# Optimization experiments

Measured on AMD Instinct MI355X. Metric: run time of the kernel, lower is better.

## Reference

```python
import jax, jax.numpy as jnp
import numpy as np

D_LATENT = 8
N_CENTERS = 48
CHANNELS = 64
PM_STEPS = 4
DT, BETA, CLAMP = 0.12, 1.0, 3.0
SIGMA_E, SIGMA_I, K_E, K_I, GAIN = 0.6, 1.2, 0.8, 1.0, 0.06


def setup_inputs() -> dict:
    key = jax.random.key(0)
    ks = jax.random.split(key, 12)
    B = 8192
    x = jax.random.normal(ks[0], (B, 784), dtype=jnp.float32)
    # encoder params (torch Linear default-ish init scale)
    W1 = jax.random.normal(ks[1], (784, 256), dtype=jnp.float32) * (1.0 / np.sqrt(784))
    b1 = jnp.zeros((256,), jnp.float32)
    W2 = jax.random.normal(ks[2], (256, D_LATENT), dtype=jnp.float32) * (1.0 / np.sqrt(256))
    b2 = jnp.zeros((D_LATENT,), jnp.float32)
    centers = jax.random.normal(ks[3], (N_CENTERS, D_LATENT), dtype=jnp.float32) * 0.7
    mus = jnp.ones((N_CENTERS,), jnp.float32) * 0.4
    projW = jax.random.normal(ks[4], (D_LATENT, CHANNELS), dtype=jnp.float32) * (1.0 / np.sqrt(D_LATENT))
    projb = jnp.zeros((CHANNELS,), jnp.float32)
    roW = jax.random.normal(ks[5], (CHANNELS, 10), dtype=jnp.float32) * (1.0 / np.sqrt(CHANNELS))
    rob = jnp.zeros((10,), jnp.float32)
    return {"x": x, "W1": W1, "b1": b1, "W2": W2, "b2": b2,
            "centers": centers, "mus": mus, "projW": projW, "projb": projb,
            "roW": roW, "rob": rob, "T": 5}


def _pm_field(z, centers, mus):
    # one PMField forward: `PM_STEPS` gradient-flow steps on z [B, d]
    for _ in range(PM_STEPS):
        diff = z[:, None, :] - centers[None, :, :]            # [B, C, d]
        r2 = jnp.sum(diff * diff, axis=-1) + 1e-4              # [B, C]
        r = jnp.sqrt(r2)
        n = 1.0 + jnp.sum(mus[None, :] / r, axis=1)            # [B]
        g = -jnp.sum(mus[None, :, None] * diff / (r * r2)[:, :, None], axis=1)  # [B, d]
        z = z + DT * BETA * (g / n[:, None])
        z = jnp.clip(z, -CLAMP, CLAMP)
    return z


def _lateral_ei(z, h):
    # kernel computed with no_grad in torch -> stop_gradient here
    sq = jnp.sum(z * z, axis=1)                                # [B]
    dist2 = jnp.maximum(sq[:, None] + sq[None, :] - 2.0 * (z @ z.T), 0.0)
    Ke = K_E * jnp.exp(-dist2 / (2.0 * SIGMA_E ** 2))
    Ki = K_I * jnp.exp(-dist2 / (2.0 * SIGMA_I ** 2))
    K = Ke - Ki
    K = K / (jnp.sum(K, axis=1, keepdims=True) + 1e-6)
    K = jax.lax.stop_gradient(K)
    return GAIN * (K @ h)


def reference(x, W1, b1, W2, b2, centers, mus, projW, projb, roW, rob, T):
    z = jnp.tanh(x @ W1 + b1) @ W2 + b2                        # encoder -> [B, d]
    h = jnp.zeros((x.shape[0], CHANNELS), x.dtype)
    logits = None
    for _ in range(T):
        z = _pm_field(z, centers, mus)
        h = 0.9 * h + 0.1 * jnp.tanh(z @ projW + projb)
        h = h + _lateral_ei(z, h)
        logits = h @ roW + rob
    return logits, z, h
```

## Files before the change

kernel.cpp:

```cpp
#include <hip/hip_runtime.h>
#include <hip/hip_bf16.h>
#include <math.h>

#define B_N      8192
#define IN_DIM   784
#define HID      256
#define DL       8
#define NC       48
#define CH       64
#define NCLS     10
#define T_ITERS  5
#define TILES    128

#define DT_      0.12f
#define CLAMP_   3.0f
#define GAIN_    0.06f
#define SQIL2    0.70776814f
#define ONE_BF16 0x3F80u

#if defined(__has_builtin)
#if __has_builtin(__builtin_amdgcn_exp2f)
#define EXP2(x) __builtin_amdgcn_exp2f(x)
#endif
#endif
#ifndef EXP2
#define EXP2(x) exp2f(x)
#endif

typedef __attribute__((ext_vector_type(8))) short short8v;
typedef __attribute__((ext_vector_type(4))) float f32x4;

__device__ __forceinline__ unsigned int pack_bf16_rhu(float lo, float hi) {
    unsigned int b0 = __builtin_bit_cast(unsigned int, lo);
    unsigned int b1 = __builtin_bit_cast(unsigned int, hi);
    return ((b0 + 0x8000u) >> 16) | ((b1 + 0x8000u) & 0xFFFF0000u);
}
__device__ __forceinline__ unsigned short bf16_1(float x) {
    return (unsigned short)((__builtin_bit_cast(unsigned int, x) + 0x8000u) >> 16);
}
__device__ __forceinline__ float bf16_to_f(unsigned short h) {
    return __builtin_bit_cast(float, ((unsigned int)h) << 16);
}

__device__ __forceinline__ void z_split(const float4 a, const float4 b,
                                        uint4& Whi, uint4& Wlo, unsigned int& Wc)
{
    float u[8] = {SQIL2*a.x, SQIL2*a.y, SQIL2*a.z, SQIL2*a.w,
                  SQIL2*b.x, SQIL2*b.y, SQIL2*b.z, SQIL2*b.w};
    float sq = 0.f;
    #pragma unroll
    for (int d = 0; d < 8; ++d) sq = fmaf(u[d], u[d], sq);
    float cn = -0.5f * sq;
    unsigned short hi[8]; float lo[8];
    #pragma unroll
    for (int d = 0; d < 8; ++d) {
        hi[d] = bf16_1(u[d]);
        lo[d] = u[d] - bf16_to_f(hi[d]);
    }
    unsigned short ch_ = bf16_1(cn);
    unsigned short cl_ = bf16_1(cn - bf16_to_f(ch_));
    Whi.x = (unsigned int)hi[0] | ((unsigned int)hi[1] << 16);
    Whi.y = (unsigned int)hi[2] | ((unsigned int)hi[3] << 16);
    Whi.z = (unsigned int)hi[4] | ((unsigned int)hi[5] << 16);
    Whi.w = (unsigned int)hi[6] | ((unsigned int)hi[7] << 16);
    Wlo.x = pack_bf16_rhu(lo[0], lo[1]); Wlo.y = pack_bf16_rhu(lo[2], lo[3]);
    Wlo.z = pack_bf16_rhu(lo[4], lo[5]); Wlo.w = pack_bf16_rhu(lo[6], lo[7]);
    Wc = (unsigned int)ch_ | ((unsigned int)cl_ << 16);
}

__global__ __launch_bounds__(256) void k_gemm1_tanh(
    const float* __restrict__ x, const float* __restrict__ W1,
    const float* __restrict__ b1, float* __restrict__ H1)
{
    __shared__ float As[2][16][68];
    __shared__ float Bs[2][16][64];
    const int tid = threadIdx.x;
    const int row0 = blockIdx.x * 64;
    const int col0 = blockIdx.y * 64;
    const int tr = tid >> 4, tc = tid & 15;
    const int am = tid >> 2, akq = tid & 3;
    const int bkk = tid >> 4, bn4 = tid & 15;
    float acc[4][4] = {};

    {
        float4 va = *(const float4*)(x + (size_t)(row0 + am) * IN_DIM + akq * 4);
        float4 vb = *(const float4*)(W1 + (size_t)bkk * HID + col0 + bn4 * 4);
        As[0][akq*4+0][am] = va.x; As[0][akq*4+1][am] = va.y;
        As[0][akq*4+2][am] = va.z; As[0][akq*4+3][am] = va.w;
        *(float4*)(&Bs[0][bkk][bn4*4]) = vb;
    }

    const int NK = IN_DIM / 16;
    #pragma unroll 1
    for (int ks = 0; ks < NK; ++ks) {
        const int cur = ks & 1;
        const bool more = (ks + 1 < NK);
        float4 va, vb;
        if (more) {
            const int k0 = (ks + 1) * 16;
            va = *(const float4*)(x + (size_t)(row0 + am) * IN_DIM + k0 + akq * 4);
            vb = *(const float4*)(W1 + (size_t)(k0 + bkk) * HID + col0 + bn4 * 4);
        }
        __syncthreads();
        #pragma unroll
        for (int kk = 0; kk < 16; ++kk) {
            float4 a = *(const float4*)(&As[cur][kk][tr*4]);
            float4 b = *(const float4*)(&Bs[cur][kk][tc*4]);
            float av[4] = {a.x, a.y, a.z, a.w};
            float bv[4] = {b.x, b.y, b.z, b.w};
            #pragma unroll
            for (int i = 0; i < 4; ++i)
                #pragma unroll
                for (int j = 0; j < 4; ++j)
                    acc[i][j] += av[i] * bv[j];
        }
        if (more) {
            const int nb = cur ^ 1;
            As[nb][akq*4+0][am] = va.x; As[nb][akq*4+1][am] = va.y;
            As[nb][akq*4+2][am] = va.z; As[nb][akq*4+3][am] = va.w;
            *(float4*)(&Bs[nb][bkk][bn4*4]) = vb;
        }
    }

    const float4 b1c = *(const float4*)(b1 + col0 + tc * 4);
    const float bb[4] = {b1c.x, b1c.y, b1c.z, b1c.w};
    #pragma unroll
    for (int i = 0; i < 4; ++i) {
        int r = row0 + tr*4 + i;
        float4 hv;
        hv.x = tanhf(acc[i][0] + bb[0]);
        hv.y = tanhf(acc[i][1] + bb[1]);
        hv.z = tanhf(acc[i][2] + bb[2]);
        hv.w = tanhf(acc[i][3] + bb[3]);
        *(float4*)(H1 + (size_t)r * HID + col0 + tc * 4) = hv;
    }
}

__global__ __launch_bounds__(256) void k_gemm2(
    const float* __restrict__ H1, const float* __restrict__ W2,
    const float* __restrict__ b2, float* __restrict__ zbuf)
{
    __shared__ float W2s[HID][DL];
    const int tid = threadIdx.x;
    for (int l = tid; l < HID * DL; l += 256) W2s[l >> 3][l & 7] = W2[l];
    __syncthreads();
    const int row = blockIdx.x * 32 + (tid >> 3);
    const int d = tid & 7;
    float acc = b2[d];
    const float* hr = H1 + (size_t)row * HID;
    for (int k = 0; k < HID; k += 4) {
        float4 hv = *(const float4*)(hr + k);
        acc += hv.x * W2s[k][d] + hv.y * W2s[k+1][d]
             + hv.z * W2s[k+2][d] + hv.w * W2s[k+3][d];
    }
    zbuf[(size_t)row * DL + d] = acc;
}

template<int S, bool HP>
__global__ __launch_bounds__(256) void k_pm_proj(
    const float* __restrict__ centers, const float* __restrict__ mus,
    const float* __restrict__ projW, const float* __restrict__ projb,
    float* __restrict__ zbuf, float* __restrict__ hB,
    unsigned short* __restrict__ hTb,
    const float* __restrict__ pAcc, const float* __restrict__ pDen)
{
    __shared__ float4 cs4[NC][2];
    __shared__ float mu_s[NC];
    __shared__ float pW[DL][CH];
    __shared__ float pb[CH];
    const int tid = threadIdx.x;
    for (int l = tid; l < NC * 2; l += 256) cs4[l >> 1][l & 1] = ((const float4*)centers)[l];
    if (tid < NC) mu_s[tid] = mus[tid];
    for (int l = tid; l < DL * CH; l += 256) pW[l >> 6][l & 63] = projW[l];
    if (tid < CH) pb[tid] = projb[tid];
    __syncthreads();

    const int rloc = tid >> 4;
    const int ln   = tid & 15;
    const int row  = blockIdx.x * 16 + rloc;

    float4 cza[3], czb[3];
    float mur[3];
    #pragma unroll
    for (int k = 0; k < 3; ++k) {
        cza[k] = cs4[ln + 16*k][0];
        czb[k] = cs4[ln + 16*k][1];
        mur[k] = mu_s[ln + 16*k];
    }

    float z[8];
    {
        const float4* zp = (const float4*)(zbuf + (size_t)row * DL);
        float4 a = zp[0], b = zp[1];
        z[0]=a.x; z[1]=a.y; z[2]=a.z; z[3]=a.w;
        z[4]=b.x; z[5]=b.y; z[6]=b.z; z[7]=b.w;
    }

    #pragma unroll
    for (int step = 0; step < 4; ++step) {
        float np = 0.f;
        float gp[8] = {0,0,0,0,0,0,0,0};
        #pragma unroll
        for (int k = 0; k < 3; ++k) {
            float d0 = z[0]-cza[k].x, d1 = z[1]-cza[k].y;
            float d2 = z[2]-cza[k].z, d3 = z[3]-cza[k].w;
            float d4 = z[4]-czb[k].x, d5 = z[5]-czb[k].y;
            float d6 = z[6]-czb[k].z, d7 = z[7]-czb[k].w;
            float r2 = 1e-4f;
            r2 = fmaf(d0,d0,r2); r2 = fmaf(d1,d1,r2);
            r2 = fmaf(d2,d2,r2); r2 = fmaf(d3,d3,r2);
            r2 = fmaf(d4,d4,r2); r2 = fmaf(d5,d5,r2);
            r2 = fmaf(d6,d6,r2); r2 = fmaf(d7,d7,r2);
            float r = sqrtf(r2);
            float mr = mur[k] / r;
            np += mr;
            float t = mr / r2;
            gp[0] = fmaf(-t, d0, gp[0]); gp[1] = fmaf(-t, d1, gp[1]);
            gp[2] = fmaf(-t, d2, gp[2]); gp[3] = fmaf(-t, d3, gp[3]);
            gp[4] = fmaf(-t, d4, gp[4]); gp[5] = fmaf(-t, d5, gp[5]);
            gp[6] = fmaf(-t, d6, gp[6]); gp[7] = fmaf(-t, d7, gp[7]);
        }
        #pragma unroll
        for (int m = 1; m < 16; m <<= 1) {
            np += __shfl_xor(np, m);
            #pragma unroll
            for (int d = 0; d < 8; ++d) gp[d] += __shfl_xor(gp[d], m);
        }
        float s = DT_ / (1.f + np);
        #pragma unroll
        for (int d = 0; d < 8; ++d) {
            z[d] = fmaf(s, gp[d], z[d]);
            z[d] = fminf(fmaxf(z[d], -CLAMP_), CLAMP_);
        }
    }

    if (ln < 8) {
        float zout = z[0];
        #pragma unroll
        for (int d = 1; d < 8; ++d) zout = (ln == d) ? z[d] : zout;
        zbuf[(size_t)row * DL + ln] = zout;
    }

    const int c0 = ln * 4;
    float hin[4];
    if (HP) {
        float den = 1e-6f;
        #pragma unroll
        for (int s = 0; s < S; ++s) den += pDen[s * B_N + row];
        float inv = GAIN_ / den;
        float4 a = {0.f, 0.f, 0.f, 0.f};
        #pragma unroll
        for (int s = 0; s < S; ++s) {
            float4 p = *(const float4*)(pAcc + (size_t)s * B_N * CH
                                        + (size_t)row * CH + c0);
            a.x += p.x; a.y += p.y; a.z += p.z; a.w += p.w;
        }
        float4 hm = *(const float4*)(hB + (size_t)row * CH + c0);
        hin[0] = fmaf(inv, a.x, hm.x);
        hin[1] = fmaf(inv, a.y, hm.y);
        hin[2] = fmaf(inv, a.z, hm.z);
        hin[3] = fmaf(inv, a.w, hm.w);
    } else {
        #pragma unroll
        for (int k = 0; k < 4; ++k) hin[k] = 0.f;
    }
    #pragma unroll
    for (int k = 0; k < 4; ++k) {
        int c = c0 + k;
        float s = pb[c];
        #pragma unroll
        for (int dd = 0; dd < DL; ++dd) s = fmaf(z[dd], pW[dd][c], s);
        hin[k] = 0.9f * hin[k] + 0.1f * tanhf(s);
    }
    float4 o0 = {hin[0], hin[1], hin[2], hin[3]};
    *(float4*)(hB + (size_t)row * CH + c0) = o0;

    {
        const int jl = row & 63;
        const int colp = (jl & 35) | ((jl & 12) << 1) | ((jl & 16) >> 2);
        const size_t tb = (size_t)(row & ~63) + colp;
        #pragma unroll
        for (int k = 0; k < 4; ++k)
            hTb[(size_t)(c0 + k) * B_N + tb] = bf16_1(hin[k]);
    }
}

template<int S>
__global__ __launch_bounds__(256, 4) void k_lateral(
    const float* __restrict__ zbuf, const unsigned short* __restrict__ hTb,
    float* __restrict__ pAcc, float* __restrict__ pDen)
{
    __shared__ __align__(16) unsigned short zA[2][64 * 24];
    __shared__ __align__(16) unsigned short hsT[2][CH][72];
    const int tid  = threadIdx.x;
    const int lane = tid & 63;
    const int wv   = tid >> 6;
    const int l15  = lane & 15;
    const int g    = lane >> 4;
    const int rowbase = blockIdx.x * 64;
    const int t0 = (TILES * blockIdx.y) / S;
    const int t1 = (TILES * (blockIdx.y + 1)) / S;
    const int chS = tid >> 2, segS = tid & 3;

    short8v bZ;
    {
        const int irow = rowbase + 16 * wv + l15;
        const float4* zp = (const float4*)(zbuf + (size_t)irow * DL);
        uint4 Whi, Wlo; unsigned int Wc;
        z_split(zp[0], zp[1], Whi, Wlo, Wc);
        union { unsigned int u[4]; short8v v; } uh, ul, ua;
        uh.u[0]=Whi.x; uh.u[1]=Whi.y; uh.u[2]=Whi.z; uh.u[3]=Whi.w;
        ul.u[0]=Wlo.x; ul.u[1]=Wlo.y; ul.u[2]=Wlo.z; ul.u[3]=Wlo.w;
        ua.u[0] = ONE_BF16 | (ONE_BF16 << 16);
        ua.u[1] = Wc; ua.u[2] = 0; ua.u[3] = 0;
        bZ = (g == 2) ? ul.v : ((g == 3) ? ua.v : uh.v);
    }
    const int offsh = (g == 1) ? 8 : ((g == 3) ? 16 : 0);

    short8v bones;
    {
        union { unsigned int u[4]; short8v v; } uo;
        uo.u[0] = uo.u[1] = uo.u[2] = uo.u[3] = ONE_BF16 | (ONE_BF16 << 16);
        bones = uo.v;
    }

    f32x4 acc0 = {0,0,0,0}, acc1 = {0,0,0,0}, acc2 = {0,0,0,0}, acc3 = {0,0,0,0};
    f32x4 acc4 = {0,0,0,0};
    const f32x4 zc = {0,0,0,0};

    {
        const int jb = t0 * 64;
        if (tid < 64) {
            const float4* zp = (const float4*)(zbuf + (size_t)(jb + tid) * DL);
            uint4 Whi, Wlo; unsigned int Wc;
            z_split(zp[0], zp[1], Whi, Wlo, Wc);
            uint4 W2v; W2v.x = Wc; W2v.y = ONE_BF16 | (ONE_BF16 << 16);
            W2v.z = 0; W2v.w = 0;
            unsigned short* dst = &zA[0][tid * 24];
            *(uint4*)(dst)      = Whi;
            *(uint4*)(dst + 8)  = Wlo;
            *(uint4*)(dst + 16) = W2v;
        }
        const unsigned short* hs = hTb + (size_t)chS * B_N + jb + segS * 16;
        *(uint4*)(&hsT[0][chS][segS * 16])     = *(const uint4*)(hs);
        *(uint4*)(&hsT[0][chS][segS * 16 + 8]) = *(const uint4*)(hs + 8);
    }

    #pragma unroll 1
    for (int jt = t0; jt < t1; ++jt) {
        const int cur = (jt - t0) & 1;
        const bool more = (jt + 1 < t1);
        uint4 h0n, h1n;
        float4 zna, znb;
        if (more) {
            const int jb2 = (jt + 1) * 64;
            const unsigned short* hs = hTb + (size_t)chS * B_N + jb2 + segS * 16;
            h0n = *(const uint4*)(hs);
            h1n = *(const uint4*)(hs + 8);
            if (tid < 64) {
                const float4* zp = (const float4*)(zbuf + (size_t)(jb2 + tid) * DL);
                zna = zp[0]; znb = zp[1];
            }
        }
        __syncthreads();

        f32x4 gac[4];
        __builtin_amdgcn_s_setprio(1);
        #pragma unroll
        for (int t = 0; t < 4; ++t) {
            short8v az = *(const short8v*)(&zA[cur][(t * 16 + l15) * 24 + offsh]);
            gac[t] = __builtin_amdgcn_mfma_f32_16x16x32_bf16(az, bZ, zc, 0, 0, 0);
        }
        __builtin_amdgcn_s_setprio(0);

        short8v afr[2];
        #pragma unroll
        for (int kb = 0; kb < 2; ++kb) {
            float w8[8];
            #pragma unroll
            for (int m = 0; m < 8; ++m) {
                float out = gac[2 * kb + (m >> 2)][m & 3];
                float e1 = EXP2(out);
                float e2 = e1 * e1;
                float e4 = e2 * e2;
                float e8 = e4 * e4;
                w8[m] = fmaf(0.8f, e8, -e2);
            }
            union { unsigned int u[4]; short8v v; } uf;
            uf.u[0] = pack_bf16_rhu(w8[0], w8[1]);
            uf.u[1] = pack_bf16_rhu(w8[2], w8[3]);
            uf.u[2] = pack_bf16_rhu(w8[4], w8[5]);
            uf.u[3] = pack_bf16_rhu(w8[6], w8[7]);
            afr[kb] = uf.v;
        }

        __builtin_amdgcn_s_setprio(1);
        #pragma unroll
        for (int kb = 0; kb < 2; ++kb) {
            const int jo = kb * 32 + g * 8;
            short8v b0 = *(const short8v*)&hsT[cur][ 0 + l15][jo];
            short8v b1 = *(const short8v*)&hsT[cur][16 + l15][jo];
            short8v b2 = *(const short8v*)&hsT[cur][32 + l15][jo];
            short8v b3 = *(const short8v*)&hsT[cur][48 + l15][jo];
            acc0 = __builtin_amdgcn_mfma_f32_16x16x32_bf16(afr[kb], b0, acc0, 0, 0, 0);
            acc1 = __builtin_amdgcn_mfma_f32_16x16x32_bf16(afr[kb], b1, acc1, 0, 0, 0);
            acc2 = __builtin_amdgcn_mfma_f32_16x16x32_bf16(afr[kb], b2, acc2, 0, 0, 0);
            acc3 = __builtin_amdgcn_mfma_f32_16x16x32_bf16(afr[kb], b3, acc3, 0, 0, 0);
            acc4 = __builtin_amdgcn_mfma_f32_16x16x32_bf16(afr[kb], bones, acc4, 0, 0, 0);
        }
        __builtin_amdgcn_s_setprio(0);

        if (more) {
            const int nb = cur ^ 1;
            if (tid < 64) {
                uint4 Whi, Wlo; unsigned int Wc;
                z_split(zna, znb, Whi, Wlo, Wc);
                uint4 W2v; W2v.x = Wc; W2v.y = ONE_BF16 | (ONE_BF16 << 16);
                W2v.z = 0; W2v.w = 0;
                unsigned short* dst = &zA[nb][tid * 24];
                *(uint4*)(dst)      = Whi;
                *(uint4*)(dst + 8)  = Wlo;
                *(uint4*)(dst + 16) = W2v;
            }
            *(uint4*)(&hsT[nb][chS][segS * 16])     = h0n;
            *(uint4*)(&hsT[nb][chS][segS * 16 + 8]) = h1n;
        }
    }

    float* pA = pAcc + (size_t)blockIdx.y * (B_N * CH) + (size_t)rowbase * CH;
    #pragma unroll
    for (int r = 0; r < 4; ++r) {
        int gi = 16 * wv + g * 4 + r;
        pA[(size_t)gi * CH +  0 + l15] = acc0[r];
        pA[(size_t)gi * CH + 16 + l15] = acc1[r];
        pA[(size_t)gi * CH + 32 + l15] = acc2[r];
        pA[(size_t)gi * CH + 48 + l15] = acc3[r];
    }
    if (l15 == 0) {
        #pragma unroll
        for (int r = 0; r < 4; ++r)
            pDen[blockIdx.y * B_N + rowbase + 16 * wv + g * 4 + r] = acc4[r];
    }
}

template<int S>
__global__ __launch_bounds__(256) void k_logits_h(
    const float* __restrict__ hmid, const float* __restrict__ pAcc,
    const float* __restrict__ pDen, const float* __restrict__ roW,
    const float* __restrict__ rob, float* __restrict__ out_logits,
    float* __restrict__ out_h)
{
    __shared__ float hsh[64][68];
    __shared__ float ro[CH][NCLS];
    __shared__ float rb[NCLS];
    const int tid = threadIdx.x;
    for (int l = tid; l < CH * NCLS; l += 256) ro[l / NCLS][l % NCLS] = roW[l];
    if (tid < NCLS) rb[tid] = rob[tid];
    const int rowbase = blockIdx.x * 64;
    const int r  = tid >> 2;
    const int c0 = (tid & 3) * 16;
    const int row = rowbase + r;
    float den = 1e-6f;
    #pragma unroll
    for (int s = 0; s < S; ++s) den += pDen[s * B_N + row];
    float inv = GAIN_ / den;
    #pragma unroll
    for (int q = 0; q < 4; ++q) {
        float4 a = {0.f, 0.f, 0.f, 0.f};
        #pragma unroll
        for (int s = 0; s < S; ++s) {
            float4 p = *(const float4*)(pAcc + (size_t)s * B_N * CH
                                        + (size_t)row * CH + c0 + q * 4);
            a.x += p.x; a.y += p.y; a.z += p.z; a.w += p.w;
        }
        float4 hm = *(const float4*)(hmid + (size_t)row * CH + c0 + q * 4);
        float4 hv;
        hv.x = fmaf(inv, a.x, hm.x); hv.y = fmaf(inv, a.y, hm.y);
        hv.z = fmaf(inv, a.z, hm.z); hv.w = fmaf(inv, a.w, hm.w);
        *(float4*)(&hsh[r][c0 + q * 4]) = hv;
        *(float4*)(out_h + (size_t)row * CH + c0 + q * 4) = hv;
    }
    __syncthreads();
    for (int idx = tid; idx < 64 * NCLS; idx += 256) {
        int rr = idx / NCLS, o = idx % NCLS;
        float s = rb[o];
        #pragma unroll
        for (int k = 0; k < CH; ++k) s = fmaf(hsh[rr][k], ro[k][o], s);
        out_logits[(size_t)(rowbase + rr) * NCLS + o] = s;
    }
}

template<int S>
static void run_all(const float* x, const float* W1, const float* b1,
                    const float* W2, const float* b2, const float* centers,
                    const float* mus, const float* projW, const float* projb,
                    const float* roW, const float* rob,
                    float* ws, float* out, hipStream_t stream)
{
    float* pAcc = ws;
    float* pDen = ws + (size_t)S * B_N * CH;
    float* zbuf = pDen + (size_t)S * B_N;
    float* hB   = zbuf + B_N * DL;
    unsigned short* hTb = (unsigned short*)(hB + B_N * CH);
    float* H1   = ws;

    float* out_logits = out;
    float* out_z      = out + 81920;
    float* out_h      = out_z + 65536;

    k_gemm1_tanh<<<dim3(B_N / 64, HID / 64), 256, 0, stream>>>(x, W1, b1, H1);
    k_gemm2<<<B_N / 32, 256, 0, stream>>>(H1, W2, b2, zbuf);

    for (int t = 0; t < T_ITERS; ++t) {
        if (t == 0)
            k_pm_proj<S, false><<<B_N / 16, 256, 0, stream>>>(
                centers, mus, projW, projb, zbuf, hB, hTb, pAcc, pDen);
        else
            k_pm_proj<S, true><<<B_N / 16, 256, 0, stream>>>(
                centers, mus, projW, projb, zbuf, hB, hTb, pAcc, pDen);
        k_lateral<S><<<dim3(TILES, S), 256, 0, stream>>>(zbuf, hTb, pAcc, pDen);
    }

    k_logits_h<S><<<TILES, 256, 0, stream>>>(hB, pAcc, pDen, roW, rob,
                                             out_logits, out_h);
    hipMemcpyAsync(out_z, zbuf, (size_t)B_N * DL * sizeof(float),
                   hipMemcpyDeviceToDevice, stream);
}

extern "C" void kernel_launch(void* const* d_in, const int* in_sizes, int n_in,
                              void* d_out, int out_size, void* d_ws, size_t ws_size,
                              hipStream_t stream)
{
    const float* x       = (const float*)d_in[0];
    const float* W1      = (const float*)d_in[1];
    const float* b1      = (const float*)d_in[2];
    const float* W2      = (const float*)d_in[3];
    const float* b2      = (const float*)d_in[4];
    const float* centers = (const float*)d_in[5];
    const float* mus     = (const float*)d_in[6];
    const float* projW   = (const float*)d_in[7];
    const float* projb   = (const float*)d_in[8];
    const float* roW     = (const float*)d_in[9];
    const float* rob     = (const float*)d_in[10];

    float* ws  = (float*)d_ws;
    float* out = (float*)d_out;

    const size_t needS8 = ((size_t)8*B_N*CH + 8*B_N + B_N*DL + B_N*CH + B_N*CH/2) * 4;
    const size_t needS4 = ((size_t)4*B_N*CH + 4*B_N + B_N*DL + B_N*CH + B_N*CH/2) * 4;

    if (ws_size >= needS8)
        run_all<8>(x, W1, b1, W2, b2, centers, mus, projW, projb, roW, rob, ws, out, stream);
    else if (ws_size >= needS4)
        run_all<4>(x, W1, b1, W2, b2, centers, mus, projW, projb, roW, rob, ws, out, stream);
    else
        run_all<2>(x, W1, b1, W2, b2, centers, mus, projW, projb, roW, rob, ws, out, stream);
}
```

Before: 297.0 us.

## Run encoder GEMM on bf16 MFMA with three-way split emulating fp32

The first encoder GEMM (x @ W1 + tanh) moves from a scalar fp32 FMA tile loop to bf16 MFMA 16x16x32 instructions. Each fp32 operand is split into three bf16 parts (hi/mid/lo), and six cross products are accumulated to keep near-fp32 accuracy. A new pre-pass kernel splits and transposes W1 into padded K-major bf16 arrays in the workspace. The change adds an extra launch, extra workspace, and per-tile splitting of x on the fly, all aimed at cutting the cost of the large GEMM.

```diff
diff --git a/kernel.cpp b/kernel.cpp
--- a/kernel.cpp
+++ b/kernel.cpp
@@ -4,6 +4,7 @@
 
 #define B_N      8192
 #define IN_DIM   784
+#define KPAD     800
 #define HID      256
 #define DL       8
 #define NC       48
@@ -68,71 +69,149 @@
     Wc = (unsigned int)ch_ | ((unsigned int)cl_ << 16);
 }
 
-__global__ __launch_bounds__(256) void k_gemm1_tanh(
-    const float* __restrict__ x, const float* __restrict__ W1,
+__device__ __forceinline__ void split3_8(const float v[8],
+                                         uint4& Th, uint4& Tm, uint4& Tl)
+{
+    unsigned short h8[8], m8[8], l8[8];
+    #pragma unroll
+    for (int d = 0; d < 8; ++d) {
+        unsigned short h = bf16_1(v[d]);
+        float r1 = v[d] - bf16_to_f(h);
+        unsigned short m = bf16_1(r1);
+        float r2 = r1 - bf16_to_f(m);
+        unsigned short l = bf16_1(r2);
+        h8[d] = h; m8[d] = m; l8[d] = l;
+    }
+    Th.x = (unsigned int)h8[0] | ((unsigned int)h8[1] << 16);
+    Th.y = (unsigned int)h8[2] | ((unsigned int)h8[3] << 16);
+    Th.z = (unsigned int)h8[4] | ((unsigned int)h8[5] << 16);
+    Th.w = (unsigned int)h8[6] | ((unsigned int)h8[7] << 16);
+    Tm.x = (unsigned int)m8[0] | ((unsigned int)m8[1] << 16);
+    Tm.y = (unsigned int)m8[2] | ((unsigned int)m8[3] << 16);
+    Tm.z = (unsigned int)m8[4] | ((unsigned int)m8[5] << 16);
+    Tm.w = (unsigned int)m8[6] | ((unsigned int)m8[7] << 16);
+    Tl.x = (unsigned int)l8[0] | ((unsigned int)l8[1] << 16);
+    Tl.y = (unsigned int)l8[2] | ((unsigned int)l8[3] << 16);
+    Tl.z = (unsigned int)l8[4] | ((unsigned int)l8[5] << 16);
+    Tl.w = (unsigned int)l8[6] | ((unsigned int)l8[7] << 16);
+}
+
+__global__ __launch_bounds__(256) void k_w1split(
+    const float* __restrict__ W1, unsigned short* __restrict__ W1aT,
+    unsigned short* __restrict__ W1bT, unsigned short* __restrict__ W1cT)
+{
+    const int k = blockIdx.x;
+    const int n = threadIdx.x;
+    float v = (k < IN_DIM) ? W1[(size_t)k * HID + n] : 0.f;
+    unsigned short h = bf16_1(v);
+    float r1 = v - bf16_to_f(h);
+    unsigned short m = bf16_1(r1);
+    unsigned short l = bf16_1(r1 - bf16_to_f(m));
+    W1aT[(size_t)n * KPAD + k] = h;
+    W1bT[(size_t)n * KPAD + k] = m;
+    W1cT[(size_t)n * KPAD + k] = l;
+}
+
+__global__ __launch_bounds__(256, 2) void k_gemm1_tanh(
+    const float* __restrict__ x, const unsigned short* __restrict__ W1aT,
+    const unsigned short* __restrict__ W1bT, const unsigned short* __restrict__ W1cT,
     const float* __restrict__ b1, float* __restrict__ H1)
 {
-    __shared__ float As[2][16][68];
-    __shared__ float Bs[2][16][64];
+    __shared__ __align__(16) unsigned short Ah[2][64][40], Am[2][64][40], Al[2][64][40];
+    __shared__ __align__(16) unsigned short Bh[2][64][40], Bm[2][64][40], Bl[2][64][40];
     const int tid = threadIdx.x;
     const int row0 = blockIdx.x * 64;
     const int col0 = blockIdx.y * 64;
-    const int tr = tid >> 4, tc = tid & 15;
-    const int am = tid >> 2, akq = tid & 3;
-    const int bkk = tid >> 4, bn4 = tid & 15;
-    float acc[4][4] = {};
+    const int wv = tid >> 6, lane = tid & 63;
+    const int l15 = lane & 15, g = lane >> 4;
+    const int sr = tid >> 2, ss = tid & 3;
+
+    f32x4 acc[4] = {{0,0,0,0},{0,0,0,0},{0,0,0,0},{0,0,0,0}};
 
     {
-        float4 va = *(const float4*)(x + (size_t)(row0 + am) * IN_DIM + akq * 4);
-        float4 vb = *(const float4*)(W1 + (size_t)bkk * HID + col0 + bn4 * 4);
-        As[0][akq*4+0][am] = va.x; As[0][akq*4+1][am] = va.y;
-        As[0][akq*4+2][am] = va.z; As[0][akq*4+3][am] = va.w;
-        *(float4*)(&Bs[0][bkk][bn4*4]) = vb;
-    }
-
-    const int NK = IN_DIM / 16;
+        float xv[8];
+        {
+            const float* xp = x + (size_t)(row0 + sr) * IN_DIM + ss * 8;
+            float4 a = *(const float4*)(xp), b = *(const float4*)(xp + 4);
+            xv[0]=a.x; xv[1]=a.y; xv[2]=a.z; xv[3]=a.w;
+            xv[4]=b.x; xv[5]=b.y; xv[6]=b.z; xv[7]=b.w;
+        }
+        uint4 Th, Tm, Tl;
+        split3_8(xv, Th, Tm, Tl);
+        *(uint4*)&Ah[0][sr][ss * 8] = Th;
+        *(uint4*)&Am[0][sr][ss * 8] = Tm;
+        *(uint4*)&Al[0][sr][ss * 8] = Tl;
+        const size_t wo = (size_t)(col0 + sr) * KPAD + ss * 8;
+        *(uint4*)&Bh[0][sr][ss * 8] = *(const uint4*)(W1aT + wo);
+        *(uint4*)&Bm[0][sr][ss * 8] = *(const uint4*)(W1bT + wo);
+        *(uint4*)&Bl[0][sr][ss * 8] = *(const uint4*)(W1cT + wo);
+    }
+
+    const int NK = KPAD / 32;
     #pragma unroll 1
     for (int ks = 0; ks < NK; ++ks) {
         const int cur = ks & 1;
         const bool more = (ks + 1 < NK);
-        float4 va, vb;
+        float xv[8];
+        uint4 wa4, wb4, wc4;
         if (more) {
-            const int k0 = (ks + 1) * 16;
-            va = *(const float4*)(x + (size_t)(row0 + am) * IN_DIM + k0 + akq * 4);
-            vb = *(const float4*)(W1 + (size_t)(k0 + bkk) * HID + col0 + bn4 * 4);
+            const int k0 = (ks + 1) * 32;
+            if (k0 + ss * 8 < IN_DIM) {
+                const float* xp = x + (size_t)(row0 + sr) * IN_DIM + k0 + ss * 8;
+                float4 a = *(const float4*)(xp), b = *(const float4*)(xp + 4);
+                xv[0]=a.x; xv[1]=a.y; xv[2]=a.z; xv[3]=a.w;
+                xv[4]=b.x; xv[5]=b.y; xv[6]=b.z; xv[7]=b.w;
+            } else {
+                #pragma unroll
+                for (int d = 0; d < 8; ++d) xv[d] = 0.f;
+            }
+            const size_t wo = (size_t)(col0 + sr) * KPAD + k0 + ss * 8;
+            wa4 = *(const uint4*)(W1aT + wo);
+            wb4 = *(const uint4*)(W1bT + wo);
+            wc4 = *(const uint4*)(W1cT + wo);
         }
         __syncthreads();
-        #pragma unroll
-        for (int kk = 0; kk < 16; ++kk) {
-            float4 a = *(const float4*)(&As[cur][kk][tr*4]);
-            float4 b = *(const float4*)(&Bs[cur][kk][tc*4]);
-            float av[4] = {a.x, a.y, a.z, a.w};
-            float bv[4] = {b.x, b.y, b.z, b.w};
-            #pragma unroll
-            for (int i = 0; i < 4; ++i)
-                #pragma unroll
-                for (int j = 0; j < 4; ++j)
-                    acc[i][j] += av[i] * bv[j];
-        }
+
+        short8v ah = *(const short8v*)&Ah[cur][16 * wv + l15][g * 8];
+        short8v am = *(const short8v*)&Am[cur][16 * wv + l15][g * 8];
+        short8v al = *(const short8v*)&Al[cur][16 * wv + l15][g * 8];
+        __builtin_amdgcn_s_setprio(1);
+        #pragma unroll
+        for (int nt = 0; nt < 4; ++nt) {
+            short8v bh = *(const short8v*)&Bh[cur][nt * 16 + l15][g * 8];
+            short8v bm = *(const short8v*)&Bm[cur][nt * 16 + l15][g * 8];
+            short8v bl = *(const short8v*)&Bl[cur][nt * 16 + l15][g * 8];
+            acc[nt] = __builtin_amdgcn_mfma_f32_16x16x32_bf16(ah, bh, acc[nt], 0, 0, 0);
+            acc[nt] = __builtin_amdgcn_mfma_f32_16x16x32_bf16(am, bh, acc[nt], 0, 0, 0);
+            acc[nt] = __builtin_amdgcn_mfma_f32_16x16x32_bf16(ah, bm, acc[nt], 0, 0, 0);
+            acc[nt] = __builtin_amdgcn_mfma_f32_16x16x32_bf16(al, bh, acc[nt], 0, 0, 0);
+            acc[nt] = __builtin_amdgcn_mfma_f32_16x16x32_bf16(am, bm, acc[nt], 0, 0, 0);
+            acc[nt] = __builtin_amdgcn_mfma_f32_16x16x32_bf16(ah, bl, acc[nt], 0, 0, 0);
+        }
+        __builtin_amdgcn_s_setprio(0);
+
         if (more) {
             const int nb = cur ^ 1;
-            As[nb][akq*4+0][am] = va.x; As[nb][akq*4+1][am] = va.y;
-            As[nb][akq*4+2][am] = va.z; As[nb][akq*4+3][am] = va.w;
-            *(float4*)(&Bs[nb][bkk][bn4*4]) = vb;
-        }
-    }
-
-    const float4 b1c = *(const float4*)(b1 + col0 + tc * 4);
-    const float bb[4] = {b1c.x, b1c.y, b1c.z, b1c.w};
-    #pragma unroll
-    for (int i = 0; i < 4; ++i) {
-        int r = row0 + tr*4 + i;
-        float4 hv;
-        hv.x = tanhf(acc[i][0] + bb[0]);
-        hv.y = tanhf(acc[i][1] + bb[1]);
-        hv.z = tanhf(acc[i][2] + bb[2]);
-        hv.w = tanhf(acc[i][3] + bb[3]);
-        *(float4*)(H1 + (size_t)r * HID + col0 + tc * 4) = hv;
+            uint4 Th, Tm, Tl;
+            split3_8(xv, Th, Tm, Tl);
+            *(uint4*)&Ah[nb][sr][ss * 8] = Th;
+            *(uint4*)&Am[nb][sr][ss * 8] = Tm;
+            *(uint4*)&Al[nb][sr][ss * 8] = Tl;
+            *(uint4*)&Bh[nb][sr][ss * 8] = wa4;
+            *(uint4*)&Bm[nb][sr][ss * 8] = wb4;
+            *(uint4*)&Bl[nb][sr][ss * 8] = wc4;
+        }
+    }
+
+    #pragma unroll
+    for (int nt = 0; nt < 4; ++nt) {
+        const int cc = col0 + nt * 16 + l15;
+        const float bc = b1[cc];
+        #pragma unroll
+        for (int r = 0; r < 4; ++r) {
+            const int rr = row0 + 16 * wv + g * 4 + r;
+            H1[(size_t)rr * HID + cc] = tanhf(acc[nt][r] + bc);
+        }
     }
 }
 
@@ -501,14 +580,18 @@
     float* pDen = ws + (size_t)S * B_N * CH;
     float* zbuf = pDen + (size_t)S * B_N;
     float* hB   = zbuf + B_N * DL;
-    unsigned short* hTb = (unsigned short*)(hB + B_N * CH);
+    unsigned short* hTb  = (unsigned short*)(hB + B_N * CH);
+    unsigned short* W1aT = hTb + (size_t)B_N * CH;
+    unsigned short* W1bT = W1aT + (size_t)HID * KPAD;
+    unsigned short* W1cT = W1bT + (size_t)HID * KPAD;
     float* H1   = ws;
 
     float* out_logits = out;
     float* out_z      = out + 81920;
     float* out_h      = out_z + 65536;
 
-    k_gemm1_tanh<<<dim3(B_N / 64, HID / 64), 256, 0, stream>>>(x, W1, b1, H1);
+    k_w1split<<<KPAD, HID, 0, stream>>>(W1, W1aT, W1bT, W1cT);
+    k_gemm1_tanh<<<dim3(B_N / 64, HID / 64), 256, 0, stream>>>(x, W1aT, W1bT, W1cT, b1, H1);
     k_gemm2<<<B_N / 32, 256, 0, stream>>>(H1, W2, b2, zbuf);
 
     for (int t = 0; t < T_ITERS; ++t) {
@@ -546,8 +629,9 @@
     float* ws  = (float*)d_ws;
     float* out = (float*)d_out;
 
-    const size_t needS8 = ((size_t)8*B_N*CH + 8*B_N + B_N*DL + B_N*CH + B_N*CH/2) * 4;
-    const size_t needS4 = ((size_t)4*B_N*CH + 4*B_N + B_N*DL + B_N*CH + B_N*CH/2) * 4;
+    const size_t extraW = (size_t)3 * HID * KPAD / 2;
+    const size_t needS8 = ((size_t)8*B_N*CH + 8*B_N + B_N*DL + B_N*CH + B_N*CH/2 + extraW) * 4;
+    const size_t needS4 = ((size_t)4*B_N*CH + 4*B_N + B_N*DL + B_N*CH + B_N*CH/2 + extraW) * 4;
 
     if (ws_size >= needS8)
         run_all<8>(x, W1, b1, W2, b2, centers, mus, projW, projb, roW, rob, ws, out, stream);
```

New measurement: 278.1 us. 6.3% less time.
